# Performance work log

Hardware: AMD Instinct MI355X
Metric: run time of the kernel (lower is better)

The kernel has to match this reference:

```python
import jax, jax.numpy as jnp
import numpy as np

B, L, D = 2, 1024, 1024
HID, E, K = 2048, 8, 2

def setup_inputs() -> dict:
    key = jax.random.key(0)
    ks = jax.random.split(key, 4)
    std = 0.02
    return {
        "x": jax.random.normal(ks[0], (B, L, D), dtype=jnp.float32),
        "router_scale": jnp.ones((D,), dtype=jnp.float32),
        "router_w": jax.random.normal(ks[1], (D, E), dtype=jnp.float32) * std,
        "gating_w": jax.random.normal(ks[2], (E, 2, HID, D), dtype=jnp.float32) * std,
        "linear_w": jax.random.normal(ks[3], (E, HID, D), dtype=jnp.float32) * std,
        "per_expert_scale": jnp.ones((E,), dtype=jnp.float32),
    }

def reference(x, router_scale, router_w, gating_w, linear_w, per_expert_scale):
    d = x.shape[-1]
    # RMSNorm without scale
    var = jnp.mean(jnp.square(x), axis=-1, keepdims=True)
    r_in = x * jax.lax.rsqrt(var + 1e-6)
    r_in = r_in * jax.lax.rsqrt(jnp.array(d, dtype=r_in.dtype)) * router_scale
    # Router
    logits = jnp.dot(r_in, router_w).astype(jnp.float32)          # [B,L,E]
    probs = jax.nn.softmax(logits, axis=-1)
    _, top_k_idx = jax.lax.top_k(logits, K)                        # [B,L,K]
    indicator = jax.nn.one_hot(top_k_idx, probs.shape[-1], dtype=probs.dtype)  # [B,L,K,E]
    gate_weights = indicator.sum(axis=-2) * probs                  # [B,L,E]
    renorm = jnp.sum(gate_weights, axis=-1, keepdims=True)
    renorm = jnp.where(renorm > 0.0, renorm, 1.0)
    weights = probs / renorm
    top_k_w = jnp.take_along_axis(weights, top_k_idx, axis=-1)     # [B,L,K]
    # Combine weights per expert (indices in top-k are distinct)
    combine = jnp.einsum('blke,blk->ble', indicator, top_k_w)      # [B,L,E]
    combine = combine * per_expert_scale                            # fold per-expert scale
    # Dense all-expert GELU-gated FFN; identical math to per-token gathered weights,
    # since unselected experts get combine weight 0.
    gate0 = jnp.einsum('bld,ehd->bleh', x, gating_w[:, 0])         # [B,L,E,H]
    gate1 = jnp.einsum('bld,ehd->bleh', x, gating_w[:, 1])
    act = jax.nn.gelu(gate0) * gate1                               # approximate gelu, as flax nn.gelu
    out = jnp.einsum('bleh,ehd,ble->bld', act, linear_w, combine)
    return out.astype(x.dtype)
```

## Files before the change

kernel.cpp:

```cpp
#include <hip/hip_runtime.h>
#include <math.h>

#define NB 2
#define NL 1024
#define ND 1024
#define NH 2048
#define NE 8
#define NTOK (NB*NL)
#define NSLOT (NTOK*2)

typedef float f32x4 __attribute__((ext_vector_type(4)));
typedef short s16x8 __attribute__((ext_vector_type(8)));
typedef short s16x4 __attribute__((ext_vector_type(4)));
typedef unsigned u32x4 __attribute__((ext_vector_type(4)));

__device__ __forceinline__ unsigned short f2bf(float f) {
    union { float f; unsigned u; } v; v.f = f;
    unsigned r = v.u + 0x7FFFu + ((v.u >> 16) & 1u);
    return (unsigned short)(r >> 16);
}

__device__ __forceinline__ unsigned pk2(float a, float b) {
    unsigned r;
    asm("v_cvt_pk_bf16_f32 %0, %1, %2" : "=v"(r) : "v"(a), "v"(b));
    return r;
}

#define SBAR() __builtin_amdgcn_sched_barrier(0)

__global__ void router_kernel(const float* __restrict__ x,
                              const float* __restrict__ rscale,
                              const float* __restrict__ rw,
                              const float* __restrict__ pes,
                              int* __restrict__ cursor,
                              int* __restrict__ tok_slot,
                              float* __restrict__ w_slot,
                              int2* __restrict__ t2s,
                              unsigned short* __restrict__ xb)
{
    const int wave = threadIdx.x >> 6;
    const int lane = threadIdx.x & 63;
    const int t = blockIdx.x * 4 + wave;
    const float* xt = x + (size_t)t * ND;
    unsigned short* xbt = xb + (size_t)t * ND;

    float part[NE];
#pragma unroll
    for (int e = 0; e < NE; ++e) part[e] = 0.f;
    float ss = 0.f;

#pragma unroll
    for (int i = 0; i < 4; ++i) {
        int d = (lane + 64 * i) * 4;
        float4 xv = *(const float4*)(xt + d);
        float4 sv = *(const float4*)(rscale + d);
        s16x4 o;
        o[0] = (short)f2bf(xv.x); o[1] = (short)f2bf(xv.y);
        o[2] = (short)f2bf(xv.z); o[3] = (short)f2bf(xv.w);
        *(s16x4*)(xbt + d) = o;
        float xs[4] = {xv.x, xv.y, xv.z, xv.w};
        float sc[4] = {sv.x, sv.y, sv.z, sv.w};
        const float* rwp = rw + (size_t)d * NE;
#pragma unroll
        for (int c = 0; c < 4; ++c) {
            float v = xs[c];
            ss += v * v;
            float xr = v * sc[c];
            float4 r0 = *(const float4*)(rwp + c * NE);
            float4 r1 = *(const float4*)(rwp + c * NE + 4);
            part[0] += xr * r0.x; part[1] += xr * r0.y;
            part[2] += xr * r0.z; part[3] += xr * r0.w;
            part[4] += xr * r1.x; part[5] += xr * r1.y;
            part[6] += xr * r1.z; part[7] += xr * r1.w;
        }
    }
#pragma unroll
    for (int off = 32; off > 0; off >>= 1) {
        ss += __shfl_xor(ss, off, 64);
#pragma unroll
        for (int e = 0; e < NE; ++e) part[e] += __shfl_xor(part[e], off, 64);
    }
    if (lane == 0) {
        float rinv = rsqrtf(ss * (1.f / ND) + 1e-6f) * rsqrtf((float)ND);
        float lg[NE];
#pragma unroll
        for (int e = 0; e < NE; ++e) lg[e] = part[e] * rinv;
        int i0 = 0; float b0 = lg[0];
#pragma unroll
        for (int e = 1; e < NE; ++e) if (lg[e] > b0) { b0 = lg[e]; i0 = e; }
        int i1 = -1; float b1 = -INFINITY;
#pragma unroll
        for (int e = 0; e < NE; ++e) if (e != i0 && lg[e] > b1) { b1 = lg[e]; i1 = e; }
        float e1 = expf(b1 - b0);
        float denom = 1.f + e1;
        float w0 = pes[i0] / denom;
        float w1 = pes[i1] * e1 / denom;
        int s0 = atomicAdd(&cursor[i0], 1);
        tok_slot[i0 * NTOK + s0] = t; w_slot[i0 * NTOK + s0] = w0;
        int s1 = atomicAdd(&cursor[i1], 1);
        tok_slot[i1 * NTOK + s1] = t; w_slot[i1 * NTOK + s1] = w1;
        t2s[t] = make_int2(i0 * NTOK + s0, i1 * NTOK + s1);
    }
}

#define TL_BLOCKS ((ND/64)*(NH/64)*NE)
__global__ __launch_bounds__(256) void prep_weights(const float* __restrict__ lw,
                                                    unsigned short* __restrict__ lwT)
{
    const int b2 = blockIdx.x;
    const int tid = threadIdx.x;
    const int d0 = (b2 & 15) * 64;
    const int h0 = ((b2 >> 4) & 31) * 64;
    const int e  = b2 >> 9;
    __shared__ unsigned short T[64][66];
    {
        const int hr = tid >> 2;
        const int dc = (tid & 3) * 16;
        const float* p = lw + ((size_t)e * NH + h0 + hr) * ND + d0 + dc;
        float t[16];
        *(float4*)&t[0]  = *(const float4*)(p);
        *(float4*)&t[4]  = *(const float4*)(p + 4);
        *(float4*)&t[8]  = *(const float4*)(p + 8);
        *(float4*)&t[12] = *(const float4*)(p + 12);
#pragma unroll
        for (int i = 0; i < 8; ++i) {
            unsigned pk = (unsigned)f2bf(t[2 * i]) | ((unsigned)f2bf(t[2 * i + 1]) << 16);
            *(unsigned*)&T[hr][dc + 2 * i] = pk;
        }
    }
    __syncthreads();
    {
        const int dr = tid >> 2;
        const int hc = (tid & 3) * 16;
        s16x8 o0, o1;
#pragma unroll
        for (int i = 0; i < 8; ++i) o0[i] = (short)T[hc + i][dr];
#pragma unroll
        for (int i = 0; i < 8; ++i) o1[i] = (short)T[hc + 8 + i][dr];
        unsigned short* q = lwT + ((size_t)e * ND + d0 + dr) * NH + h0 + hc;
        *(s16x8*)(q)     = o0;
        *(s16x8*)(q + 8) = o1;
    }
}

#define BM 128
#define BH 64
#define BK 32

#define G_ISSUE(Sa0,Sa1,Sb0,Sb1,Sb2,Sb3,k) do { \
    Sa0 = *(const s16x8*)(asrc0 + (k)); \
    Sa1 = *(const s16x8*)(asrc1 + (k)); \
    Sb0 = *(const f32x4*)(bsrc0 + (k)); \
    Sb1 = *(const f32x4*)(bsrc0 + (k) + 4); \
    Sb2 = *(const f32x4*)(bsrc1 + (k)); \
    Sb3 = *(const f32x4*)(bsrc1 + (k) + 4); \
} while(0)

#define G_WRITE(P,Sa0,Sa1,Sb0,Sb1,Sb2,Sb3) do { \
    *(s16x8*)&As[P][arow][acol]      = Sa0; \
    *(s16x8*)&As[P][arow + 16][acol] = Sa1; \
    u32x4 w0_, w1_; \
    w0_[0] = pk2(Sb0[0],Sb0[1]); w0_[1] = pk2(Sb0[2],Sb0[3]); \
    w0_[2] = pk2(Sb1[0],Sb1[1]); w0_[3] = pk2(Sb1[2],Sb1[3]); \
    w1_[0] = pk2(Sb2[0],Sb2[1]); w1_[1] = pk2(Sb2[2],Sb2[3]); \
    w1_[2] = pk2(Sb3[0],Sb3[1]); w1_[3] = pk2(Sb3[2],Sb3[3]); \
    *(u32x4*)&Bs[P][arow][acol]      = w0_; \
    *(u32x4*)&Bs[P][arow + 16][acol] = w1_; \
} while(0)

#define G_COMPUTE(P) do { \
    s16x8 af[4], bfr[2][2]; \
    _Pragma("unroll") \
    for (int i_ = 0; i_ < 4; ++i_) \
        af[i_] = *(const s16x8*)&As[P][wm * 64 + i_ * 16 + fr][pS]; \
    _Pragma("unroll") \
    for (int g_ = 0; g_ < 2; ++g_) \
        _Pragma("unroll") \
        for (int j_ = 0; j_ < 2; ++j_) \
            bfr[g_][j_] = *(const s16x8*)&Bs[P][g_ * 64 + wn * 32 + j_ * 16 + fr][pS]; \
    _Pragma("unroll") \
    for (int g_ = 0; g_ < 2; ++g_) \
        _Pragma("unroll") \
        for (int i_ = 0; i_ < 4; ++i_) \
            _Pragma("unroll") \
            for (int j_ = 0; j_ < 2; ++j_) \
                acc[g_][i_][j_] = __builtin_amdgcn_mfma_f32_16x16x32_bf16( \
                    af[i_], bfr[g_][j_], acc[g_][i_][j_], 0, 0, 0); \
} while(0)

__global__ __launch_bounds__(256, 3) void gate_gemm(
    const unsigned short* __restrict__ xb, const float* __restrict__ gw,
    const int* __restrict__ cursor,
    const int* __restrict__ tok_slot, const float* __restrict__ w_slot,
    unsigned short* __restrict__ act)
{
    const int e = blockIdx.z;
    const int n = cursor[e];
    const int row0 = blockIdx.y * BM;
    if (row0 >= n) return;
    const int b0 = e * NTOK;
    const int h0 = blockIdx.x * BH;

    __shared__ unsigned short As[2][BM][BK];
    __shared__ unsigned short Bs[2][BM][BK];
    __shared__ int toks[BM];
    __shared__ float swv[BM];

    const int tid = threadIdx.x;
    if (tid < BM) {
        int r = row0 + tid;
        toks[tid] = (r < n) ? tok_slot[b0 + r] : 0;
        swv[tid]  = (r < n) ? w_slot[b0 + r] : 0.f;
    }
    __syncthreads();

    const int lane = tid & 63;
    const int wid  = tid >> 6;
    const int wm = wid & 1;
    const int wn = wid >> 1;

    const int drow = lane >> 2;
    const int c8  = (((lane & 3) - ((lane >> 3) & 3)) & 3) * 8;
    const int arow = wid * 32 + drow;
    const int acol = (lane & 3) * 8;
    const unsigned short* asrc0 = xb + (size_t)toks[arow] * ND + c8;
    const unsigned short* asrc1 = xb + (size_t)toks[arow + 16] * ND + c8;
    const int br1 = arow + 16;
    const float* bsrc0 = gw + (((size_t)e * 2 + (arow >> 6)) * NH + h0 + (arow & 63)) * ND + c8;
    const float* bsrc1 = gw + (((size_t)e * 2 + (br1 >> 6)) * NH + h0 + (br1 & 63)) * ND + c8;

    f32x4 acc[2][4][2];
#pragma unroll
    for (int gg = 0; gg < 2; ++gg)
#pragma unroll
        for (int i = 0; i < 4; ++i)
#pragma unroll
            for (int j = 0; j < 2; ++j)
                acc[gg][i][j] = (f32x4){0.f, 0.f, 0.f, 0.f};

    const int fr = lane & 15;
    const int pS = (((lane >> 4) + (fr >> 1)) & 3) * 8;

    const int NT = ND / BK;

    s16x8 xa0, xa1, ya0, ya1;
    f32x4 xb0, xb1, xb2, xb3, yb0, yb1, yb2, yb3;

    G_ISSUE(xa0, xa1, xb0, xb1, xb2, xb3, 0);
    G_ISSUE(ya0, ya1, yb0, yb1, yb2, yb3, BK);
    SBAR();
    G_WRITE(0, xa0, xa1, xb0, xb1, xb2, xb3);
    __syncthreads();

    for (int t = 0; t < NT; t += 2) {
        if (t + 2 < NT) G_ISSUE(xa0, xa1, xb0, xb1, xb2, xb3, (t + 2) * BK);
        SBAR();
        G_COMPUTE(0);
        SBAR();
        G_WRITE(1, ya0, ya1, yb0, yb1, yb2, yb3);
        __syncthreads();
        if (t + 3 < NT) G_ISSUE(ya0, ya1, yb0, yb1, yb2, yb3, (t + 3) * BK);
        SBAR();
        G_COMPUTE(1);
        SBAR();
        if (t + 2 < NT) G_WRITE(0, xa0, xa1, xb0, xb1, xb2, xb3);
        __syncthreads();
    }

    const int rb = (lane >> 4) * 4;
#pragma unroll
    for (int i = 0; i < 4; ++i)
#pragma unroll
        for (int r = 0; r < 4; ++r) {
            int ml = wm * 64 + i * 16 + rb + r;
            int rr = row0 + ml;
            if (rr < n) {
                float w = swv[ml];
#pragma unroll
                for (int j = 0; j < 2; ++j) {
                    float g0v = acc[0][i][j][r];
                    float g1v = acc[1][i][j][r];
                    float u = 0.7978845608028654f * (g0v + 0.044715f * g0v * g0v * g0v);
                    float ex = __expf(2.f * u);
                    float th = 1.f - 2.f / (ex + 1.f);
                    float a = 0.5f * g0v * (1.f + th) * g1v * w;
                    act[(size_t)(b0 + rr) * NH + (h0 + wn * 32 + j * 16 + fr)] = f2bf(a);
                }
            }
        }
}

#define DBM 128
#define DBN 128
#define DBK 32
#define KSPLIT 2
#define KC (NH / KSPLIT)

#define D_ISSUE(Sa0,Sa1,Sb0,Sb1,k) do { \
    Sa0 = *(const s16x8*)(asrc0 + (k)); \
    Sa1 = *(const s16x8*)(asrc1 + (k)); \
    Sb0 = *(const s16x8*)(bsrc0 + (k)); \
    Sb1 = *(const s16x8*)(bsrc1 + (k)); \
} while(0)

#define D_WRITE(P,Sa0,Sa1,Sb0,Sb1) do { \
    *(s16x8*)&As[P][arow][acol]      = Sa0; \
    *(s16x8*)&As[P][arow + 16][acol] = Sa1; \
    *(s16x8*)&Bs[P][arow][acol]      = Sb0; \
    *(s16x8*)&Bs[P][arow + 16][acol] = Sb1; \
} while(0)

#define D_COMPUTE(P) do { \
    s16x8 af[4], bfr[4]; \
    _Pragma("unroll") \
    for (int i_ = 0; i_ < 4; ++i_) \
        af[i_] = *(const s16x8*)&As[P][wm * 64 + i_ * 16 + fr][pS]; \
    _Pragma("unroll") \
    for (int j_ = 0; j_ < 4; ++j_) \
        bfr[j_] = *(const s16x8*)&Bs[P][wn * 64 + j_ * 16 + fr][pS]; \
    _Pragma("unroll") \
    for (int i_ = 0; i_ < 4; ++i_) \
        _Pragma("unroll") \
        for (int j_ = 0; j_ < 4; ++j_) \
            acc[i_][j_] = __builtin_amdgcn_mfma_f32_16x16x32_bf16( \
                af[i_], bfr[j_], acc[i_][j_], 0, 0, 0); \
} while(0)

__global__ __launch_bounds__(256, 3) void down_gemm(
    const unsigned short* __restrict__ act, const unsigned short* __restrict__ lwT,
    const int* __restrict__ cursor,
    const int* __restrict__ tok_slot, float* __restrict__ partial)
{
    const int e  = blockIdx.z >> 1;
    const int kc = blockIdx.z & 1;
    const int n = cursor[e];
    const int row0 = blockIdx.y * DBM;
    if (row0 >= n) return;
    const int b0 = e * NTOK;
    const int d0 = blockIdx.x * DBN;

    __shared__ unsigned short As[2][DBM][DBK];
    __shared__ unsigned short Bs[2][DBN][DBK];

    const int tid = threadIdx.x;
    const int lane = tid & 63;
    const int wid  = tid >> 6;
    const int wm = wid & 1;
    const int wn = wid >> 1;

    const int drow = lane >> 2;
    const int c8  = (((lane & 3) - ((lane >> 3) & 3)) & 3) * 8;
    const int arow = wid * 32 + drow;
    const int acol = (lane & 3) * 8;
    const int rr0 = row0 + arow, rr1 = rr0 + 16;
    const int sl0 = b0 + (rr0 < n ? rr0 : 0);
    const int sl1 = b0 + (rr1 < n ? rr1 : 0);
    const unsigned short* asrc0 = act + (size_t)sl0 * NH + kc * KC + c8;
    const unsigned short* asrc1 = act + (size_t)sl1 * NH + kc * KC + c8;
    const unsigned short* bsrc0 = lwT + ((size_t)e * ND + d0 + arow) * NH + kc * KC + c8;
    const unsigned short* bsrc1 = bsrc0 + 16 * NH;

    f32x4 acc[4][4];
#pragma unroll
    for (int i = 0; i < 4; ++i)
#pragma unroll
        for (int j = 0; j < 4; ++j)
            acc[i][j] = (f32x4){0.f, 0.f, 0.f, 0.f};

    const int fr = lane & 15;
    const int pS = (((lane >> 4) + (fr >> 1)) & 3) * 8;

    const int NT = KC / DBK;

    s16x8 xa0, xa1, xb0, xb1;
    s16x8 ya0, ya1, yb0, yb1;

    D_ISSUE(xa0, xa1, xb0, xb1, 0);
    D_ISSUE(ya0, ya1, yb0, yb1, DBK);
    SBAR();
    D_WRITE(0, xa0, xa1, xb0, xb1);
    __syncthreads();

    for (int t = 0; t < NT; t += 2) {
        if (t + 2 < NT) D_ISSUE(xa0, xa1, xb0, xb1, (t + 2) * DBK);
        SBAR();
        D_COMPUTE(0);
        SBAR();
        D_WRITE(1, ya0, ya1, yb0, yb1);
        __syncthreads();
        if (t + 3 < NT) D_ISSUE(ya0, ya1, yb0, yb1, (t + 3) * DBK);
        SBAR();
        D_COMPUTE(1);
        SBAR();
        if (t + 2 < NT) D_WRITE(0, xa0, xa1, xb0, xb1);
        __syncthreads();
    }

    float* prt = partial + ((size_t)kc * (NE * NTOK)) * ND;
    const int rb = (lane >> 4) * 4;
#pragma unroll
    for (int i = 0; i < 4; ++i)
#pragma unroll
        for (int r = 0; r < 4; ++r) {
            int ml = wm * 64 + i * 16 + rb + r;
            int rr = row0 + ml;
            if (rr < n) {
#pragma unroll
                for (int j = 0; j < 4; ++j)
                    prt[(size_t)(b0 + rr) * ND + d0 + wn * 64 + j * 16 + fr] = acc[i][j][r];
            }
        }
}

__global__ __launch_bounds__(256) void gather_out(const float* __restrict__ partial,
                                                  const int2* __restrict__ t2s,
                                                  float* __restrict__ out)
{
    const int t = blockIdx.x;
    const int2 ss = t2s[t];
    const size_t plane = (size_t)(NE * NTOK) * ND;
    const float* p00 = partial + (size_t)ss.x * ND;
    const float* p01 = p00 + plane;
    const float* p10 = partial + (size_t)ss.y * ND;
    const float* p11 = p10 + plane;
    const int d = threadIdx.x * 4;
    f32x4 a = *(const f32x4*)(p00 + d);
    f32x4 b = *(const f32x4*)(p01 + d);
    f32x4 c = *(const f32x4*)(p10 + d);
    f32x4 e = *(const f32x4*)(p11 + d);
    f32x4 v = a + b + c + e;
    *(f32x4*)(out + (size_t)t * ND + d) = v;
}

extern "C" void kernel_launch(void* const* d_in, const int* in_sizes, int n_in,
                              void* d_out, int out_size, void* d_ws, size_t ws_size,
                              hipStream_t stream)
{
    const float* x      = (const float*)d_in[0];
    const float* rscale = (const float*)d_in[1];
    const float* rw     = (const float*)d_in[2];
    const float* gw     = (const float*)d_in[3];
    const float* lw     = (const float*)d_in[4];
    const float* pes    = (const float*)d_in[5];
    float* out = (float*)d_out;

    char* ws = (char*)d_ws;
    int* cursor = (int*)ws;
    int*   tok_slot      = (int*)(ws + 128);
    float* w_slot        = (float*)(ws + 65664);
    int2*  t2s           = (int2*)(ws + 131200);
    unsigned short* xb   = (unsigned short*)(ws + 147584);
    unsigned short* act  = (unsigned short*)(ws + 4341888);
    unsigned short* lwT  = (unsigned short*)(ws + 71450752);
    float* partial       = (float*)(ws + 105005184);

    hipMemsetAsync(d_ws, 0, 128, stream);

    router_kernel<<<NTOK / 4, 256, 0, stream>>>(x, rscale, rw, pes, cursor,
                                                tok_slot, w_slot, t2s, xb);

    prep_weights<<<TL_BLOCKS, 256, 0, stream>>>(lw, lwT);

    dim3 g2(NH / BH, NTOK / BM, NE);
    gate_gemm<<<g2, 256, 0, stream>>>(xb, gw, cursor, tok_slot, w_slot, act);

    dim3 g3(ND / DBN, NTOK / DBM, NE * KSPLIT);
    down_gemm<<<g3, 256, 0, stream>>>(act, lwT, cursor, tok_slot, partial);

    gather_out<<<NTOK, 256, 0, stream>>>(partial, t2s, out);
}
```

Baseline: 403.6 us.

## Stage GEMM operands via direct global-to-LDS loads with triple-buffered pipeline

Both expert GEMMs now load bf16 operand tiles straight into shared memory with global_load_lds instead of going through registers and ds_write. The gate GEMM still converts the fp32 weights through registers, but its loads use explicit inline asm with manual vmcnt waits. The down GEMM moves to a three-stage LDS ring with one barrier per K-step, so a further load can be in flight while the current tile is computed. The intent is to cut register pressure and LDS write instructions and to overlap more memory traffic. In exchange there is more LDS use, fragile hand-written waitcnt logic, and a possible layout mismatch with the swizzled read pattern.

```diff
diff --git a/kernel.cpp b/kernel.cpp
--- a/kernel.cpp
+++ b/kernel.cpp
@@ -20,13 +20,28 @@
     return (unsigned short)(r >> 16);
 }
 
-__device__ __forceinline__ unsigned pk2(float a, float b) {
+__device__ __forceinline__ unsigned pk2v(float a, float b) {
     unsigned r;
-    asm("v_cvt_pk_bf16_f32 %0, %1, %2" : "=v"(r) : "v"(a), "v"(b));
+    asm volatile("v_cvt_pk_bf16_f32 %0, %1, %2" : "=v"(r) : "v"(a), "v"(b));
     return r;
 }
 
+__device__ __forceinline__ void gld4(f32x4& d, const float* p) {
+    asm volatile("global_load_dwordx4 %0, %1, off" : "=&v"(d) : "v"(p));
+}
+
+__device__ __forceinline__ void gl_lds16(const unsigned short* g, unsigned short* l) {
+    __builtin_amdgcn_global_load_lds(
+        (const __attribute__((address_space(1))) unsigned int*)(const void*)g,
+        (__attribute__((address_space(3))) unsigned int*)(void*)l, 16, 0, 0);
+}
+
 #define SBAR() __builtin_amdgcn_sched_barrier(0)
+#define VMW(N) do { asm volatile("s_waitcnt vmcnt(" #N ")" ::: "memory"); SBAR(); } while(0)
+#define WAVE_SYNC() do { \
+    asm volatile("s_waitcnt lgkmcnt(0)" ::: "memory"); \
+    __builtin_amdgcn_s_barrier(); SBAR(); } while(0)
+#define BAR() do { __builtin_amdgcn_s_barrier(); SBAR(); } while(0)
 
 __global__ void router_kernel(const float* __restrict__ x,
                               const float* __restrict__ rscale,
@@ -147,23 +162,12 @@
 #define BH 64
 #define BK 32
 
-#define G_ISSUE(Sa0,Sa1,Sb0,Sb1,Sb2,Sb3,k) do { \
-    Sa0 = *(const s16x8*)(asrc0 + (k)); \
-    Sa1 = *(const s16x8*)(asrc1 + (k)); \
-    Sb0 = *(const f32x4*)(bsrc0 + (k)); \
-    Sb1 = *(const f32x4*)(bsrc0 + (k) + 4); \
-    Sb2 = *(const f32x4*)(bsrc1 + (k)); \
-    Sb3 = *(const f32x4*)(bsrc1 + (k) + 4); \
-} while(0)
-
-#define G_WRITE(P,Sa0,Sa1,Sb0,Sb1,Sb2,Sb3) do { \
-    *(s16x8*)&As[P][arow][acol]      = Sa0; \
-    *(s16x8*)&As[P][arow + 16][acol] = Sa1; \
+#define G_WRITE(P,B0,B1,B2,B3) do { \
     u32x4 w0_, w1_; \
-    w0_[0] = pk2(Sb0[0],Sb0[1]); w0_[1] = pk2(Sb0[2],Sb0[3]); \
-    w0_[2] = pk2(Sb1[0],Sb1[1]); w0_[3] = pk2(Sb1[2],Sb1[3]); \
-    w1_[0] = pk2(Sb2[0],Sb2[1]); w1_[1] = pk2(Sb2[2],Sb2[3]); \
-    w1_[2] = pk2(Sb3[0],Sb3[1]); w1_[3] = pk2(Sb3[2],Sb3[3]); \
+    w0_[0] = pk2v(B0[0],B0[1]); w0_[1] = pk2v(B0[2],B0[3]); \
+    w0_[2] = pk2v(B1[0],B1[1]); w0_[3] = pk2v(B1[2],B1[3]); \
+    w1_[0] = pk2v(B2[0],B2[1]); w1_[1] = pk2v(B2[2],B2[3]); \
+    w1_[2] = pk2v(B3[0],B3[1]); w1_[3] = pk2v(B3[2],B3[3]); \
     *(u32x4*)&Bs[P][arow][acol]      = w0_; \
     *(u32x4*)&Bs[P][arow + 16][acol] = w1_; \
 } while(0)
@@ -186,6 +190,11 @@
             for (int j_ = 0; j_ < 2; ++j_) \
                 acc[g_][i_][j_] = __builtin_amdgcn_mfma_f32_16x16x32_bf16( \
                     af[i_], bfr[g_][j_], acc[g_][i_][j_], 0, 0, 0); \
+} while(0)
+
+#define GLD_B(B0,B1,B2,B3,k) do { \
+    gld4(B0, bsrc0 + (k)); gld4(B1, bsrc0 + (k) + 4); \
+    gld4(B2, bsrc1 + (k)); gld4(B3, bsrc1 + (k) + 4); \
 } while(0)
 
 __global__ __launch_bounds__(256, 3) void gate_gemm(
@@ -243,28 +252,43 @@
 
     const int NT = ND / BK;
 
-    s16x8 xa0, xa1, ya0, ya1;
-    f32x4 xb0, xb1, xb2, xb3, yb0, yb1, yb2, yb3;
-
-    G_ISSUE(xa0, xa1, xb0, xb1, xb2, xb3, 0);
-    G_ISSUE(ya0, ya1, yb0, yb1, yb2, yb3, BK);
+    f32x4 Xb0, Xb1, Xb2, Xb3;
+    f32x4 Yb0, Yb1, Yb2, Yb3;
+
+    gl_lds16(asrc0, &As[0][wid * 32][0]);
+    gl_lds16(asrc1, &As[0][wid * 32 + 16][0]);
     SBAR();
-    G_WRITE(0, xa0, xa1, xb0, xb1, xb2, xb3);
-    __syncthreads();
+    GLD_B(Xb0, Xb1, Xb2, Xb3, 0);
+    GLD_B(Yb0, Yb1, Yb2, Yb3, BK);
+    VMW(4);
+    G_WRITE(0, Xb0, Xb1, Xb2, Xb3);
+    WAVE_SYNC();
 
     for (int t = 0; t < NT; t += 2) {
-        if (t + 2 < NT) G_ISSUE(xa0, xa1, xb0, xb1, xb2, xb3, (t + 2) * BK);
+        if (t + 1 < NT) {
+            gl_lds16(asrc0 + (t + 1) * BK, &As[1][wid * 32][0]);
+            gl_lds16(asrc1 + (t + 1) * BK, &As[1][wid * 32 + 16][0]);
+        }
         SBAR();
+        if (t + 2 < NT) GLD_B(Xb0, Xb1, Xb2, Xb3, (t + 2) * BK);
         G_COMPUTE(0);
-        SBAR();
-        G_WRITE(1, ya0, ya1, yb0, yb1, yb2, yb3);
-        __syncthreads();
-        if (t + 3 < NT) G_ISSUE(ya0, ya1, yb0, yb1, yb2, yb3, (t + 3) * BK);
-        SBAR();
-        G_COMPUTE(1);
-        SBAR();
-        if (t + 2 < NT) G_WRITE(0, xa0, xa1, xb0, xb1, xb2, xb3);
-        __syncthreads();
+        if (t + 2 < NT) { VMW(4); } else { VMW(0); }
+        if (t + 1 < NT) {
+            G_WRITE(1, Yb0, Yb1, Yb2, Yb3);
+            WAVE_SYNC();
+            if (t + 2 < NT) {
+                gl_lds16(asrc0 + (t + 2) * BK, &As[0][wid * 32][0]);
+                gl_lds16(asrc1 + (t + 2) * BK, &As[0][wid * 32 + 16][0]);
+            }
+            SBAR();
+            if (t + 3 < NT) GLD_B(Yb0, Yb1, Yb2, Yb3, (t + 3) * BK);
+            G_COMPUTE(1);
+            if (t + 3 < NT) { VMW(4); } else if (t + 2 < NT) { VMW(0); }
+            if (t + 2 < NT) {
+                G_WRITE(0, Xb0, Xb1, Xb2, Xb3);
+                WAVE_SYNC();
+            }
+        }
     }
 
     const int rb = (lane >> 4) * 4;
@@ -296,18 +320,11 @@
 #define KSPLIT 2
 #define KC (NH / KSPLIT)
 
-#define D_ISSUE(Sa0,Sa1,Sb0,Sb1,k) do { \
-    Sa0 = *(const s16x8*)(asrc0 + (k)); \
-    Sa1 = *(const s16x8*)(asrc1 + (k)); \
-    Sb0 = *(const s16x8*)(bsrc0 + (k)); \
-    Sb1 = *(const s16x8*)(bsrc1 + (k)); \
-} while(0)
-
-#define D_WRITE(P,Sa0,Sa1,Sb0,Sb1) do { \
-    *(s16x8*)&As[P][arow][acol]      = Sa0; \
-    *(s16x8*)&As[P][arow + 16][acol] = Sa1; \
-    *(s16x8*)&Bs[P][arow][acol]      = Sb0; \
-    *(s16x8*)&Bs[P][arow + 16][acol] = Sb1; \
+#define D_STAGE(b, k) do { \
+    gl_lds16(asrc0 + (k), &As[b][wid * 32][0]); \
+    gl_lds16(asrc1 + (k), &As[b][wid * 32 + 16][0]); \
+    gl_lds16(bsrc0 + (k), &Bs[b][wid * 32][0]); \
+    gl_lds16(bsrc1 + (k), &Bs[b][wid * 32 + 16][0]); \
 } while(0)
 
 #define D_COMPUTE(P) do { \
@@ -339,10 +356,17 @@
     const int b0 = e * NTOK;
     const int d0 = blockIdx.x * DBN;
 
-    __shared__ unsigned short As[2][DBM][DBK];
-    __shared__ unsigned short Bs[2][DBN][DBK];
+    __shared__ unsigned short As[3][DBM][DBK];
+    __shared__ unsigned short Bs[3][DBM][DBK];
+    __shared__ int stok[DBM];
 
     const int tid = threadIdx.x;
+    if (tid < DBM) {
+        int r = row0 + tid;
+        stok[tid] = (r < n) ? tok_slot[b0 + r] : 0;
+    }
+    __syncthreads();
+
     const int lane = tid & 63;
     const int wid  = tid >> 6;
     const int wm = wid & 1;
@@ -351,7 +375,6 @@
     const int drow = lane >> 2;
     const int c8  = (((lane & 3) - ((lane >> 3) & 3)) & 3) * 8;
     const int arow = wid * 32 + drow;
-    const int acol = (lane & 3) * 8;
     const int rr0 = row0 + arow, rr1 = rr0 + 16;
     const int sl0 = b0 + (rr0 < n ? rr0 : 0);
     const int sl1 = b0 + (rr1 < n ? rr1 : 0);
@@ -372,28 +395,22 @@
 
     const int NT = KC / DBK;
 
-    s16x8 xa0, xa1, xb0, xb1;
-    s16x8 ya0, ya1, yb0, yb1;
-
-    D_ISSUE(xa0, xa1, xb0, xb1, 0);
-    D_ISSUE(ya0, ya1, yb0, yb1, DBK);
+    D_STAGE(0, 0);
     SBAR();
-    D_WRITE(0, xa0, xa1, xb0, xb1);
-    __syncthreads();
-
-    for (int t = 0; t < NT; t += 2) {
-        if (t + 2 < NT) D_ISSUE(xa0, xa1, xb0, xb1, (t + 2) * DBK);
+    D_STAGE(1, DBK);
+    VMW(4);
+    BAR();
+
+    int bc = 0;
+    for (int t = 0; t < NT; ++t) {
+        int b2 = bc + 2; if (b2 >= 3) b2 -= 3;
+        if (t + 2 < NT) D_STAGE(b2, (t + 2) * DBK);
         SBAR();
-        D_COMPUTE(0);
-        SBAR();
-        D_WRITE(1, ya0, ya1, yb0, yb1);
-        __syncthreads();
-        if (t + 3 < NT) D_ISSUE(ya0, ya1, yb0, yb1, (t + 3) * DBK);
-        SBAR();
-        D_COMPUTE(1);
-        SBAR();
-        if (t + 2 < NT) D_WRITE(0, xa0, xa1, xb0, xb1);
-        __syncthreads();
+        D_COMPUTE(bc);
+        if (t + 2 < NT) { VMW(4); }
+        else if (t + 1 < NT) { VMW(0); }
+        if (t + 1 < NT) BAR();
+        bc += 1; if (bc == 3) bc = 0;
     }
 
     float* prt = partial + ((size_t)kc * (NE * NTOK)) * ND;
```

Measured after the change: 401.2 us. Within noise of the previous version (-0.6%).
